# Kernel tuning notes

Measured on AMD Instinct MI355X. Metric: run time of the kernel, lower is better.

The kernel has to match this reference:

```python
import jax, jax.numpy as jnp
import numpy as np
import math

N = 512; D = 256; L = 6; H = 8; BINS = 64; LAM = 30.0; STEPS = 8; VOCAB = 20


def _pe(n, d):
    pos = jnp.arange(n, dtype=jnp.float32)[:, None]
    div = jnp.exp(jnp.arange(0, d, 2, dtype=jnp.float32) * (-math.log(10000.0) / d))
    pe = jnp.zeros((n, d), jnp.float32)
    pe = pe.at[:, 0::2].set(jnp.sin(pos * div))
    pe = pe.at[:, 1::2].set(jnp.cos(pos * div))
    return pe


def _ln(x, g, b, eps=1e-5):
    m = x.mean(-1, keepdims=True)
    v = x.var(-1, keepdims=True)
    return (x - m) / jnp.sqrt(v + eps) * g + b


def _gelu(x):
    return jax.nn.gelu(x, approximate=False)  # torch nn.GELU default (erf)


def setup_inputs() -> dict:
    key = jax.random.key(0)
    ks = jax.random.split(key, 20)
    s = 0.02
    nrm = lambda k, sh: jax.random.normal(k, sh, jnp.float32) * s
    z = lambda sh: jnp.zeros(sh, jnp.float32)
    o = lambda sh: jnp.ones(sh, jnp.float32)
    return {
        "tokens": jax.random.randint(ks[0], (1, N), 0, VOCAB),
        "emb": nrm(ks[1], (VOCAB, D)),
        "Wqkv": nrm(ks[2], (L, 3 * D, D)), "bqkv": z((L, 3 * D)),
        "Wo": nrm(ks[3], (L, D, D)), "bo": z((L, D)),
        "g1": o((L, D)), "be1": z((L, D)),
        "W1": nrm(ks[4], (L, 4 * D, D)), "b1": z((L, 4 * D)),
        "W2": nrm(ks[5], (L, D, 4 * D)), "b2": z((L, D)),
        "g2": o((L, D)), "be2": z((L, D)),
        "A1": nrm(ks[6], (D, D)), "a1b": z((D,)),
        "A2": nrm(ks[7], (1, D)), "a2b": z((1,)),
        "Cf": nrm(ks[8], (D, D)), "cb": z((D,)),
        "F1": nrm(ks[9], (D, 2 * D)), "f1b": z((D,)),
        "F2": nrm(ks[10], (BINS, D)), "f2b": z((BINS,)),
        "T1": nrm(ks[11], (D, D)), "t1b": z((D,)),
        "T2": nrm(ks[12], (2, D)), "t2b": z((2,)),
        "Cp": nrm(ks[13], (3, D)), "cpb": z((3,)),
        "noise": jax.random.normal(ks[14], (1, N, 3), jnp.float32),
    }


def reference(tokens, emb, Wqkv, bqkv, Wo, bo, g1, be1, W1, b1, W2, b2, g2, be2,
              A1, a1b, A2, a2b, Cf, cb, F1, f1b, F2, f2b, T1, t1b, T2, t2b,
              Cp, cpb, noise):
    x = emb[tokens] + _pe(N, D)  # [1,N,D]
    dh = D // H
    for l in range(L):  # post-norm TransformerEncoderLayer, ReLU activation
        qkv = x @ Wqkv[l].T + bqkv[l]  # [1,N,3D]
        q, k, v = jnp.split(qkv, 3, axis=-1)
        q = q.reshape(1, N, H, dh).transpose(0, 2, 1, 3)
        k = k.reshape(1, N, H, dh).transpose(0, 2, 1, 3)
        v = v.reshape(1, N, H, dh).transpose(0, 2, 1, 3)
        att = jax.nn.softmax(jnp.einsum('bhqd,bhkd->bhqk', q, k) / math.sqrt(dh), axis=-1)
        o = jnp.einsum('bhqk,bhkd->bhqd', att, v).transpose(0, 2, 1, 3).reshape(1, N, D)
        x = _ln(x + o @ Wo[l].T + bo[l], g1[l], be1[l])
        f = jax.nn.relu(x @ W1[l].T + b1[l]) @ W2[l].T + b2[l]
        x = _ln(x + f, g2[l], be2[l])
    latent = x
    # AdaptiveAlphaPredictor
    ah = _gelu(latent @ A1.T + a1b) @ A2.T + a2b  # [1,N,1]
    alpha = 1.2 + jax.nn.sigmoid(ah)[..., 0] * (3.5 - 1.2)  # [1,N]
    # CSOCRGAttention: power-law x exp-decay kernel over |i-j|
    idx = jnp.arange(N, dtype=jnp.float32)
    r = jnp.abs(idx[:, None] - idx[None, :]) + 1e-4  # [N,N]
    ap = (alpha[:, :, None] + alpha[:, None, :]) * 0.5  # [1,N,N]
    kern = r[None] ** (-ap) * jnp.exp(-r[None] / LAM)
    kern = kern / (kern.sum(-1, keepdims=True) + 1e-8)
    latent = jnp.einsum('bij,bjd->bid', kern, latent)
    # ContactPriorHead
    hh = latent @ Cf.T + cb
    contact = jax.nn.sigmoid(jnp.einsum('bid,bjd->bij', hh, hh))
    # DistogramHead: cat([xi, xj]) @ F1.T == xi @ F1[:, :D].T + xj @ F1[:, D:].T
    hi = latent @ F1[:, :D].T  # [1,N,D]
    hj = latent @ F1[:, D:].T  # [1,N,D]
    ph = _gelu(hi[:, :, None, :] + hj[:, None, :, :] + f1b)  # [1,N,N,D]
    disto = ph @ F2.T + f2b  # [1,N,N,BINS]
    # TorsionGenerator
    t = _gelu(latent @ T1.T + t1b) @ T2.T + t2b  # [1,N,2]
    phi = jnp.tanh(t[..., 0]) * jnp.pi
    psi = jnp.tanh(t[..., 1]) * jnp.pi
    # DiffusionInitializer: fixed small sequential refinement loop
    target = latent @ Cp.T + cpb  # [1,N,3]
    xc = noise
    for tt in reversed(range(STEPS)):
        a = (tt + 1) / STEPS
        xc = a * xc + (1.0 - a) * target
    return latent, alpha, contact, disto, phi, psi, xc


if __name__ == "__main__":
    outs = reference(**setup_inputs())
    for o in outs:
        print(o.shape, o.dtype)
```

## Files before the change

### kernel.cpp

```cpp
#include <hip/hip_runtime.h>
#include <hip/hip_bf16.h>

#define DEV __device__ __forceinline__

typedef float f32x4 __attribute__((ext_vector_type(4)));
typedef short short8 __attribute__((ext_vector_type(8)));
typedef short short4v __attribute__((ext_vector_type(4)));

DEV short f2bf(float f) {
    union { float f; unsigned u; } c; c.f = f;
    unsigned r = (c.u + 0x7FFFu + ((c.u >> 16) & 1u)) >> 16;
    return (short)r;
}

DEV short f2bf_n(float f) {
    __hip_bfloat16 b = __float2bfloat16(f);
    union { __hip_bfloat16 b; short s; } c; c.b = b;
    return c.s;
}

DEV float gelu_t(float x) {
    float x2 = x * x;
    float y = x * (0.7978845608f + 0.0356774081f * x2);
    float e = exp2f(-2.8853900817779268f * fabsf(y));
    float t = (1.f - e) * __frcp_rn(1.f + e);
    t = copysignf(t, y);
    return 0.5f * x * (1.f + t);
}

DEV float wred_sum(float v) {
    #pragma unroll
    for (int off = 1; off < 64; off <<= 1) v += __shfl_xor(v, off);
    return v;
}

struct CvtPack {
    const float* s[9];
    short* d[9];
    int n[9];
};
__global__ __launch_bounds__(256) void k_cvt_all(CvtPack p) {
    #pragma unroll 1
    for (int seg = 0; seg < 9; ++seg) {
        int n4 = p.n[seg] >> 2;
        const float4* src = (const float4*)p.s[seg];
        short4v* dst = (short4v*)p.d[seg];
        for (int i = blockIdx.x * 256 + threadIdx.x; i < n4; i += gridDim.x * 256) {
            float4 v = src[i];
            short4v o;
            o[0] = f2bf(v.x); o[1] = f2bf(v.y); o[2] = f2bf(v.z); o[3] = f2bf(v.w);
            dst[i] = o;
        }
    }
}

__global__ __launch_bounds__(256) void k_embed(const int* __restrict__ tokens,
                                               const float* __restrict__ emb,
                                               float* __restrict__ x,
                                               short* __restrict__ xb) {
    int n = blockIdx.x, d = threadIdx.x;
    int tok = tokens[n];
    float div = expf((float)((d >> 1) * 2) * -0.035977892079030837f);
    float arg = (float)n * div;
    float pe = (d & 1) ? cosf(arg) : sinf(arg);
    float v = emb[tok * 256 + d] + pe;
    x[n * 256 + d] = v;
    xb[n * 256 + d] = f2bf(v);
}

__global__ __launch_bounds__(64) void k_gemm16(const short* __restrict__ A,
                                               const short* __restrict__ W,
                                               const float* __restrict__ bias,
                                               float* __restrict__ outf,
                                               short* __restrict__ outb,
                                               short* __restrict__ vt,
                                               int M, int K, int ldw, int act) {
    int m0 = blockIdx.x * 16, n0 = blockIdx.y * 16;
    int lane = threadIdx.x;
    int cr = lane & 15, g = lane >> 4;
    const short* a0 = A + (size_t)(n0 + cr) * K + g * 8;
    const short* b0 = W + (size_t)(m0 + cr) * ldw + g * 8;
    f32x4 acc = {0.f, 0.f, 0.f, 0.f};
    #pragma unroll 8
    for (int k = 0; k < K; k += 32) {
        short8 av = *(const short8*)(a0 + k);
        short8 bv = *(const short8*)(b0 + k);
        acc = __builtin_amdgcn_mfma_f32_16x16x32_bf16(av, bv, acc, 0, 0, 0);
    }
    float bb = bias ? bias[m0 + cr] : 0.f;
    int m = m0 + cr;
    #pragma unroll
    for (int r = 0; r < 4; ++r) {
        int row = n0 + g * 4 + r;
        float v = acc[r] + bb;
        if (act == 1) v = fmaxf(v, 0.f);
        else if (act == 2) v = gelu_t(v);
        else if (act == 3) v = 1.f / (1.f + __expf(-v));
        if (outf) outf[(size_t)row * M + m] = v;
        if (outb) outb[(size_t)row * M + m] = f2bf(v);
        if (vt && m >= 512) vt[(size_t)(m - 512) * 512 + row] = f2bf(v);
    }
}

__global__ __launch_bounds__(64) void k_attn3(const short* __restrict__ qkvb,
                                              const short* __restrict__ vt,
                                              short* __restrict__ obuf_bf) {
    __shared__ __align__(16) short Pb[16][40];
    int h = blockIdx.x, qt = blockIdx.y;
    int lane = threadIdx.x;
    int cr = lane & 15, g = lane >> 4;
    int qb = qt * 16;
    short8 qf = *(const short8*)(qkvb + (size_t)(qb + cr) * 768 + h * 32 + g * 8);
    f32x4 s[32];
    #pragma unroll
    for (int jt = 0; jt < 32; ++jt) {
        short8 kf = *(const short8*)(qkvb + (size_t)(jt * 16 + cr) * 768 + 256 + h * 32 + g * 8);
        f32x4 z = {0.f, 0.f, 0.f, 0.f};
        s[jt] = __builtin_amdgcn_mfma_f32_16x16x32_bf16(qf, kf, z, 0, 0, 0);
    }
    const float sc = 0.17677669529663687f;
    float m[4], l[4];
    #pragma unroll
    for (int r = 0; r < 4; ++r) {
        float mm = -1e30f;
        #pragma unroll
        for (int jt = 0; jt < 32; ++jt) mm = fmaxf(mm, s[jt][r]);
        #pragma unroll
        for (int off = 1; off < 16; off <<= 1) mm = fmaxf(mm, __shfl_xor(mm, off));
        m[r] = mm * sc;
    }
    #pragma unroll
    for (int r = 0; r < 4; ++r) {
        float ll = 0.f;
        #pragma unroll
        for (int jt = 0; jt < 32; ++jt) {
            float p = __expf(s[jt][r] * sc - m[r]);
            s[jt][r] = p;
            ll += p;
        }
        #pragma unroll
        for (int off = 1; off < 16; off <<= 1) ll += __shfl_xor(ll, off);
        l[r] = ll;
    }
    const short* vth0 = vt + (size_t)(h * 32 + cr) * 512;
    const short* vth1 = vt + (size_t)(h * 32 + 16 + cr) * 512;
    f32x4 o0 = {0.f,0.f,0.f,0.f}, o1 = o0;
    #pragma unroll
    for (int c = 0; c < 16; ++c) {
        #pragma unroll
        for (int r = 0; r < 4; ++r) {
            Pb[4 * g + r][cr]      = f2bf(s[2 * c][r]);
            Pb[4 * g + r][16 + cr] = f2bf(s[2 * c + 1][r]);
        }
        short8 pa = *(const short8*)&Pb[cr][g * 8];
        short8 v0 = *(const short8*)(vth0 + c * 32 + g * 8);
        short8 v1 = *(const short8*)(vth1 + c * 32 + g * 8);
        o0 = __builtin_amdgcn_mfma_f32_16x16x32_bf16(pa, v0, o0, 0, 0, 0);
        o1 = __builtin_amdgcn_mfma_f32_16x16x32_bf16(pa, v1, o1, 0, 0, 0);
    }
    #pragma unroll
    for (int r = 0; r < 4; ++r) {
        float inv = 1.f / l[r];
        int q = qb + 4 * g + r;
        short* op = obuf_bf + (size_t)q * 256 + h * 32;
        op[cr]      = f2bf(o0[r] * inv);
        op[16 + cr] = f2bf(o1[r] * inv);
    }
}

__global__ __launch_bounds__(64) void k_ln(const float* xr, const float* y,
                                           const float* __restrict__ g,
                                           const float* __restrict__ b,
                                           float* out, short* outb) {
    int n = blockIdx.x, lane = threadIdx.x;
    float4 xv = *(const float4*)(xr + (size_t)n * 256 + lane * 4);
    float4 yv = *(const float4*)(y + (size_t)n * 256 + lane * 4);
    float t0 = xv.x + yv.x, t1 = xv.y + yv.y, t2 = xv.z + yv.z, t3 = xv.w + yv.w;
    float s = t0 + t1 + t2 + t3;
    float sq = t0 * t0 + t1 * t1 + t2 * t2 + t3 * t3;
    s = wred_sum(s);
    sq = wred_sum(sq);
    float mean = s * (1.f / 256.f);
    float var = sq * (1.f / 256.f) - mean * mean;
    float rstd = rsqrtf(var + 1e-5f);
    float4 gv = *(const float4*)(g + lane * 4);
    float4 bv = *(const float4*)(b + lane * 4);
    float r0 = (t0 - mean) * rstd * gv.x + bv.x;
    float r1 = (t1 - mean) * rstd * gv.y + bv.y;
    float r2 = (t2 - mean) * rstd * gv.z + bv.z;
    float r3 = (t3 - mean) * rstd * gv.w + bv.w;
    *(float4*)(out + (size_t)n * 256 + lane * 4) = make_float4(r0, r1, r2, r3);
    short4v ob; ob[0] = f2bf(r0); ob[1] = f2bf(r1); ob[2] = f2bf(r2); ob[3] = f2bf(r3);
    *(short4v*)(outb + (size_t)n * 256 + lane * 4) = ob;
}

__global__ __launch_bounds__(64) void k_alpha(const float* __restrict__ g,
                                              const float* __restrict__ A2,
                                              const float* __restrict__ a2b,
                                              float* __restrict__ alpha) {
    int n = blockIdx.x, lane = threadIdx.x;
    float4 gv = *(const float4*)(g + (size_t)n * 256 + lane * 4);
    float4 av = *(const float4*)(A2 + lane * 4);
    float s = gv.x * av.x + gv.y * av.y + gv.z * av.z + gv.w * av.w;
    s = wred_sum(s);
    if (lane == 0) {
        float ah = s + a2b[0];
        alpha[n] = 1.2f + 2.3f / (1.f + __expf(-ah));
    }
}

__global__ __launch_bounds__(256) void k_kern(const float* __restrict__ latent,
                                              const float* __restrict__ alpha,
                                              float* __restrict__ out,
                                              short* __restrict__ outb) {
    __shared__ float wl[512];
    __shared__ float partial[4];
    int i = blockIdx.x, t = threadIdx.x;
    float ai = alpha[i];
    float w0, w1;
    {
        int j = t;
        float dd = fabsf((float)(i - j)) + 1e-4f;
        float ap = 0.5f * (ai + alpha[j]);
        w0 = exp2f(-ap * __log2f(dd) - dd * 0.048089834696298776f);
        j = t + 256;
        dd = fabsf((float)(i - j)) + 1e-4f;
        ap = 0.5f * (ai + alpha[j]);
        w1 = exp2f(-ap * __log2f(dd) - dd * 0.048089834696298776f);
    }
    wl[t] = w0; wl[t + 256] = w1;
    float s = wred_sum(w0 + w1);
    if ((t & 63) == 0) partial[t >> 6] = s;
    __syncthreads();
    float S = partial[0] + partial[1] + partial[2] + partial[3];
    float inv = 1.f / (S + 1e-8f);
    float acc = 0.f;
    #pragma unroll 4
    for (int j = 0; j < 512; ++j) acc += wl[j] * latent[(size_t)j * 256 + t];
    float v = acc * inv;
    out[(size_t)i * 256 + t] = v;
    outb[(size_t)i * 256 + t] = f2bf(v);
}

__global__ __launch_bounds__(256) void k_disto3(const float* __restrict__ hi,
                                                const float* __restrict__ hj,
                                                const short* __restrict__ F2bf,
                                                const float* __restrict__ f2b,
                                                float* __restrict__ out) {
    __shared__ __align__(16) float hjs[16][260];
    int jt = blockIdx.x, it = blockIdx.y;
    int j0 = jt * 16;
    int t = threadIdx.x;
    for (int q = t; q < 1024; q += 256) {
        int r = q >> 6, c = (q & 63) << 2;
        float4 v = *(const float4*)(hj + (size_t)(j0 + r) * 256 + c);
        *(float4*)&hjs[r][c] = v;
    }
    __syncthreads();
    int w = t >> 6, lane = t & 63;
    int cr = lane & 15, g = lane >> 4;
    int i0 = it * 8 + w * 2;
    float bb[4];
    #pragma unroll
    for (int c = 0; c < 4; ++c) bb[c] = f2b[c * 16 + cr];
    f32x4 acc[2][4];
    #pragma unroll
    for (int ii = 0; ii < 2; ++ii)
        #pragma unroll
        for (int c = 0; c < 4; ++c) acc[ii][c] = (f32x4){0.f,0.f,0.f,0.f};
    #pragma unroll 1
    for (int ks = 0; ks < 8; ++ks) {
        int kb = ks * 32 + g * 8;
        short8 B[4];
        #pragma unroll
        for (int c = 0; c < 4; ++c)
            B[c] = *(const short8*)(F2bf + (size_t)(c * 16 + cr) * 256 + kb);
        float4 ja = *(const float4*)&hjs[cr][kb];
        float4 jb = *(const float4*)&hjs[cr][kb + 4];
        #pragma unroll
        for (int ii = 0; ii < 2; ++ii) {
            const float* hr = hi + (size_t)(i0 + ii) * 256 + kb;
            float4 ha = *(const float4*)(hr);
            float4 hb = *(const float4*)(hr + 4);
            short8 af;
            af[0] = f2bf_n(gelu_t(ha.x + ja.x));
            af[1] = f2bf_n(gelu_t(ha.y + ja.y));
            af[2] = f2bf_n(gelu_t(ha.z + ja.z));
            af[3] = f2bf_n(gelu_t(ha.w + ja.w));
            af[4] = f2bf_n(gelu_t(hb.x + jb.x));
            af[5] = f2bf_n(gelu_t(hb.y + jb.y));
            af[6] = f2bf_n(gelu_t(hb.z + jb.z));
            af[7] = f2bf_n(gelu_t(hb.w + jb.w));
            #pragma unroll
            for (int c = 0; c < 4; ++c)
                acc[ii][c] = __builtin_amdgcn_mfma_f32_16x16x32_bf16(af, B[c], acc[ii][c], 0, 0, 0);
        }
    }
    #pragma unroll
    for (int ii = 0; ii < 2; ++ii) {
        #pragma unroll
        for (int r = 0; r < 4; ++r) {
            int jl = g * 4 + r;
            float* op = out + ((size_t)(i0 + ii) * 512 + j0 + jl) * 64;
            op[cr]      = acc[ii][0][r] + bb[0];
            op[cr + 16] = acc[ii][1][r] + bb[1];
            op[cr + 32] = acc[ii][2][r] + bb[2];
            op[cr + 48] = acc[ii][3][r] + bb[3];
        }
    }
}

__global__ __launch_bounds__(64) void k_torsion(const float* __restrict__ g,
                                                const float* __restrict__ T2,
                                                const float* __restrict__ t2b,
                                                float* __restrict__ phi,
                                                float* __restrict__ psi) {
    int n = blockIdx.x, lane = threadIdx.x;
    float4 gv = *(const float4*)(g + (size_t)n * 256 + lane * 4);
    float4 w0 = *(const float4*)(T2 + lane * 4);
    float4 w1 = *(const float4*)(T2 + 256 + lane * 4);
    float s0 = gv.x * w0.x + gv.y * w0.y + gv.z * w0.z + gv.w * w0.w;
    float s1 = gv.x * w1.x + gv.y * w1.y + gv.z * w1.z + gv.w * w1.w;
    s0 = wred_sum(s0);
    s1 = wred_sum(s1);
    if (lane == 0) {
        phi[n] = tanhf(s0 + t2b[0]) * 3.14159265358979323846f;
        psi[n] = tanhf(s1 + t2b[1]) * 3.14159265358979323846f;
    }
}

__global__ __launch_bounds__(64) void k_diffusion(const float* __restrict__ latent,
                                                  const float* __restrict__ Cp,
                                                  const float* __restrict__ cpb,
                                                  const float* __restrict__ noise,
                                                  float* __restrict__ xc) {
    int n = blockIdx.x, lane = threadIdx.x;
    float4 lv = *(const float4*)(latent + (size_t)n * 256 + lane * 4);
    const float CN = 40320.0f / 16777216.0f;
    float s[3];
    #pragma unroll
    for (int c = 0; c < 3; ++c) {
        float4 w = *(const float4*)(Cp + c * 256 + lane * 4);
        float v = lv.x * w.x + lv.y * w.y + lv.z * w.z + lv.w * w.w;
        s[c] = wred_sum(v);
    }
    if (lane == 0) {
        #pragma unroll
        for (int c = 0; c < 3; ++c) {
            float tg = s[c] + cpb[c];
            xc[n * 3 + c] = CN * noise[n * 3 + c] + (1.f - CN) * tg;
        }
    }
}

extern "C" void kernel_launch(void* const* d_in, const int* in_sizes, int n_in,
                              void* d_out, int out_size, void* d_ws, size_t ws_size,
                              hipStream_t stream) {
    const int*   tokens = (const int*)d_in[0];
    const float* emb  = (const float*)d_in[1];
    const float* Wqkv = (const float*)d_in[2];
    const float* bqkv = (const float*)d_in[3];
    const float* Wo   = (const float*)d_in[4];
    const float* bo   = (const float*)d_in[5];
    const float* g1   = (const float*)d_in[6];
    const float* be1  = (const float*)d_in[7];
    const float* W1   = (const float*)d_in[8];
    const float* b1   = (const float*)d_in[9];
    const float* W2   = (const float*)d_in[10];
    const float* b2   = (const float*)d_in[11];
    const float* g2   = (const float*)d_in[12];
    const float* be2  = (const float*)d_in[13];
    const float* A1   = (const float*)d_in[14];
    const float* a1b  = (const float*)d_in[15];
    const float* A2   = (const float*)d_in[16];
    const float* a2b  = (const float*)d_in[17];
    const float* Cf   = (const float*)d_in[18];
    const float* cb   = (const float*)d_in[19];
    const float* F1   = (const float*)d_in[20];
    const float* f1b  = (const float*)d_in[21];
    const float* F2   = (const float*)d_in[22];
    const float* f2b  = (const float*)d_in[23];
    const float* T1   = (const float*)d_in[24];
    const float* t1b  = (const float*)d_in[25];
    const float* T2   = (const float*)d_in[26];
    const float* t2b  = (const float*)d_in[27];
    const float* Cp   = (const float*)d_in[28];
    const float* cpb  = (const float*)d_in[29];
    const float* noise= (const float*)d_in[30];

    float* ws   = (float*)d_ws;
    float* x    = ws;
    float* y2   = ws + 131072;
    float* gbuf = ws + 262144;
    float* hi   = ws + 393216;
    float* hj   = ws + 524288;
    short* S    = (short*)(ws + 655360);
    short* x_bf    = S;
    short* obuf_bf = S + 131072;
    short* h1_bf   = S + 262144;
    short* hh_bf   = S + 786432;
    short* lat_bf  = S + 917504;
    short* F2bf    = S + 1048576;
    short* qkv_bf  = S + 1064960;
    short* vt      = S + 1458176;
    short* Wqkv_bf = S + 1589248;
    short* Wo_bf   = S + 2768896;
    short* W1_bf   = S + 3162112;
    short* W2_bf   = S + 4734976;
    short* A1_bf   = S + 6307840;
    short* Cf_bf   = S + 6373376;
    short* F1_bf   = S + 6438912;
    short* T1_bf   = S + 6569984;

    float* out = (float*)d_out;
    float* o_latent  = out;
    float* o_alpha   = out + 131072;
    float* o_contact = out + 131584;
    float* o_disto   = out + 393728;
    float* o_phi     = out + 17170944;
    float* o_psi     = out + 17171456;
    float* o_xc      = out + 17171968;

    CvtPack p;
    p.s[0] = Wqkv; p.d[0] = Wqkv_bf; p.n[0] = 1179648;
    p.s[1] = Wo;   p.d[1] = Wo_bf;   p.n[1] = 393216;
    p.s[2] = W1;   p.d[2] = W1_bf;   p.n[2] = 1572864;
    p.s[3] = W2;   p.d[3] = W2_bf;   p.n[3] = 1572864;
    p.s[4] = A1;   p.d[4] = A1_bf;   p.n[4] = 65536;
    p.s[5] = Cf;   p.d[5] = Cf_bf;   p.n[5] = 65536;
    p.s[6] = F1;   p.d[6] = F1_bf;   p.n[6] = 131072;
    p.s[7] = T1;   p.d[7] = T1_bf;   p.n[7] = 65536;
    p.s[8] = F2;   p.d[8] = F2bf;    p.n[8] = 16384;
    k_cvt_all<<<512, 256, 0, stream>>>(p);

    k_embed<<<512, 256, 0, stream>>>(tokens, emb, x, x_bf);

    for (int l = 0; l < 6; ++l) {
        k_gemm16<<<dim3(48, 32), 64, 0, stream>>>(x_bf, Wqkv_bf + (size_t)l * 196608,
            bqkv + l * 768, nullptr, qkv_bf, vt, 768, 256, 256, 0);
        k_attn3<<<dim3(8, 32), 64, 0, stream>>>(qkv_bf, vt, obuf_bf);
        k_gemm16<<<dim3(16, 32), 64, 0, stream>>>(obuf_bf, Wo_bf + (size_t)l * 65536,
            bo + l * 256, y2, nullptr, nullptr, 256, 256, 256, 0);
        k_ln<<<512, 64, 0, stream>>>(x, y2, g1 + l * 256, be1 + l * 256, x, x_bf);
        k_gemm16<<<dim3(64, 32), 64, 0, stream>>>(x_bf, W1_bf + (size_t)l * 262144,
            b1 + l * 1024, nullptr, h1_bf, nullptr, 1024, 256, 256, 1);
        k_gemm16<<<dim3(16, 32), 64, 0, stream>>>(h1_bf, W2_bf + (size_t)l * 262144,
            b2 + l * 256, y2, nullptr, nullptr, 256, 1024, 1024, 0);
        k_ln<<<512, 64, 0, stream>>>(x, y2, g2 + l * 256, be2 + l * 256, x, x_bf);
    }

    k_gemm16<<<dim3(16, 32), 64, 0, stream>>>(x_bf, A1_bf, a1b, gbuf, nullptr, nullptr,
                                              256, 256, 256, 2);
    k_alpha<<<512, 64, 0, stream>>>(gbuf, A2, a2b, o_alpha);
    k_kern<<<512, 256, 0, stream>>>(x, o_alpha, o_latent, lat_bf);
    k_gemm16<<<dim3(16, 32), 64, 0, stream>>>(lat_bf, Cf_bf, cb, nullptr, hh_bf, nullptr,
                                              256, 256, 256, 0);
    k_gemm16<<<dim3(32, 32), 64, 0, stream>>>(hh_bf, hh_bf, nullptr, o_contact, nullptr,
                                              nullptr, 512, 256, 256, 3);
    k_gemm16<<<dim3(16, 32), 64, 0, stream>>>(lat_bf, F1_bf, f1b, hi, nullptr, nullptr,
                                              256, 256, 512, 0);
    k_gemm16<<<dim3(16, 32), 64, 0, stream>>>(lat_bf, F1_bf + 256, nullptr, hj, nullptr,
                                              nullptr, 256, 256, 512, 0);
    k_disto3<<<dim3(32, 64), 256, 0, stream>>>(hi, hj, F2bf, f2b, o_disto);
    k_gemm16<<<dim3(16, 32), 64, 0, stream>>>(lat_bf, T1_bf, t1b, gbuf, nullptr, nullptr,
                                              256, 256, 256, 2);
    k_torsion<<<512, 64, 0, stream>>>(gbuf, T2, t2b, o_phi, o_psi);
    k_diffusion<<<512, 64, 0, stream>>>(o_latent, Cp, cpb, noise, o_xc);
}
```

Baseline: 389.8 us.

## Fuse Wo+LayerNorm and FFN+LayerNorm kernels, speed up GELU and bf16 packing

```diff
diff --git a/kernel.cpp b/kernel.cpp
--- a/kernel.cpp
+++ b/kernel.cpp
@@ -6,6 +6,17 @@
 typedef float f32x4 __attribute__((ext_vector_type(4)));
 typedef short short8 __attribute__((ext_vector_type(8)));
 typedef short short4v __attribute__((ext_vector_type(4)));
+
+#if __has_builtin(__builtin_amdgcn_exp2f)
+#define EXP2F __builtin_amdgcn_exp2f
+#else
+#define EXP2F exp2f
+#endif
+#if __has_builtin(__builtin_amdgcn_rcpf)
+#define RCPF __builtin_amdgcn_rcpf
+#else
+#define RCPF(x) (1.f / (x))
+#endif
 
 DEV short f2bf(float f) {
     union { float f; unsigned u; } c; c.f = f;
@@ -13,24 +24,30 @@
     return (short)r;
 }
 
-DEV short f2bf_n(float f) {
-    __hip_bfloat16 b = __float2bfloat16(f);
-    union { __hip_bfloat16 b; short s; } c; c.b = b;
-    return c.s;
-}
-
-DEV float gelu_t(float x) {
+DEV int cvt_pk_bf16(float lo, float hi) {
+    int d;
+    asm("v_cvt_pk_bf16_f32 %0, %1, %2" : "=v"(d) : "v"(lo), "v"(hi));
+    return d;
+}
+
+DEV float gelu_fast(float x) {
     float x2 = x * x;
-    float y = x * (0.7978845608f + 0.0356774081f * x2);
-    float e = exp2f(-2.8853900817779268f * fabsf(y));
-    float t = (1.f - e) * __frcp_rn(1.f + e);
-    t = copysignf(t, y);
+    float y = x * __builtin_fmaf(0.0356774081f, x2, 0.7978845608f);
+    y = fminf(fmaxf(y, -15.f), 15.f);
+    float e = EXP2F(y * 2.8853900817779268f);
+    float r = RCPF(e + 1.f);
+    float t = (e - 1.f) * r;
     return 0.5f * x * (1.f + t);
 }
 
 DEV float wred_sum(float v) {
     #pragma unroll
     for (int off = 1; off < 64; off <<= 1) v += __shfl_xor(v, off);
+    return v;
+}
+DEV float red16(float v) {
+    #pragma unroll
+    for (int off = 1; off < 16; off <<= 1) v += __shfl_xor(v, off);
     return v;
 }
 
@@ -94,7 +111,7 @@
         int row = n0 + g * 4 + r;
         float v = acc[r] + bb;
         if (act == 1) v = fmaxf(v, 0.f);
-        else if (act == 2) v = gelu_t(v);
+        else if (act == 2) v = gelu_fast(v);
         else if (act == 3) v = 1.f / (1.f + __expf(-v));
         if (outf) outf[(size_t)row * M + m] = v;
         if (outb) outb[(size_t)row * M + m] = f2bf(v);
@@ -168,30 +185,145 @@
     }
 }
 
-__global__ __launch_bounds__(64) void k_ln(const float* xr, const float* y,
-                                           const float* __restrict__ g,
-                                           const float* __restrict__ b,
-                                           float* out, short* outb) {
-    int n = blockIdx.x, lane = threadIdx.x;
-    float4 xv = *(const float4*)(xr + (size_t)n * 256 + lane * 4);
-    float4 yv = *(const float4*)(y + (size_t)n * 256 + lane * 4);
-    float t0 = xv.x + yv.x, t1 = xv.y + yv.y, t2 = xv.z + yv.z, t3 = xv.w + yv.w;
-    float s = t0 + t1 + t2 + t3;
-    float sq = t0 * t0 + t1 * t1 + t2 * t2 + t3 * t3;
-    s = wred_sum(s);
-    sq = wred_sum(sq);
-    float mean = s * (1.f / 256.f);
-    float var = sq * (1.f / 256.f) - mean * mean;
-    float rstd = rsqrtf(var + 1e-5f);
-    float4 gv = *(const float4*)(g + lane * 4);
-    float4 bv = *(const float4*)(b + lane * 4);
-    float r0 = (t0 - mean) * rstd * gv.x + bv.x;
-    float r1 = (t1 - mean) * rstd * gv.y + bv.y;
-    float r2 = (t2 - mean) * rstd * gv.z + bv.z;
-    float r3 = (t3 - mean) * rstd * gv.w + bv.w;
-    *(float4*)(out + (size_t)n * 256 + lane * 4) = make_float4(r0, r1, r2, r3);
-    short4v ob; ob[0] = f2bf(r0); ob[1] = f2bf(r1); ob[2] = f2bf(r2); ob[3] = f2bf(r3);
-    *(short4v*)(outb + (size_t)n * 256 + lane * 4) = ob;
+__global__ __launch_bounds__(512) void k_wo_ln(const short* __restrict__ obuf_bf,
+                                               const short* __restrict__ Wo_bf,
+                                               const float* __restrict__ bo,
+                                               const float* __restrict__ xres,
+                                               const float* __restrict__ gam,
+                                               const float* __restrict__ bet,
+                                               float* __restrict__ x_out,
+                                               short* __restrict__ xb_out) {
+    __shared__ float redS[16][8];
+    __shared__ float redQ[16][8];
+    int n0 = blockIdx.x * 16;
+    int t = threadIdx.x, w = t >> 6, lane = t & 63;
+    int cr = lane & 15, g = lane >> 4;
+    const short* a0 = obuf_bf + (size_t)(n0 + cr) * 256 + g * 8;
+    float tv[2][4];
+    #pragma unroll
+    for (int tt = 0; tt < 2; ++tt) {
+        int m0 = w * 32 + tt * 16;
+        const short* b0 = Wo_bf + (size_t)(m0 + cr) * 256 + g * 8;
+        f32x4 a = {0.f, 0.f, 0.f, 0.f};
+        #pragma unroll
+        for (int k = 0; k < 256; k += 32) {
+            a = __builtin_amdgcn_mfma_f32_16x16x32_bf16(*(const short8*)(a0 + k),
+                                                        *(const short8*)(b0 + k), a, 0, 0, 0);
+        }
+        float bb = bo[m0 + cr];
+        #pragma unroll
+        for (int r = 0; r < 4; ++r) {
+            int row = n0 + g * 4 + r;
+            tv[tt][r] = a[r] + bb + xres[(size_t)row * 256 + m0 + cr];
+        }
+    }
+    #pragma unroll
+    for (int r = 0; r < 4; ++r) {
+        float s = tv[0][r] + tv[1][r];
+        float q = tv[0][r] * tv[0][r] + tv[1][r] * tv[1][r];
+        s = red16(s);
+        q = red16(q);
+        if (cr == 0) { redS[g * 4 + r][w] = s; redQ[g * 4 + r][w] = q; }
+    }
+    __syncthreads();
+    #pragma unroll
+    for (int r = 0; r < 4; ++r) {
+        int row = g * 4 + r;
+        float S = 0.f, Q = 0.f;
+        #pragma unroll
+        for (int j = 0; j < 8; ++j) { S += redS[row][j]; Q += redQ[row][j]; }
+        float mean = S * (1.f / 256.f);
+        float var = Q * (1.f / 256.f) - mean * mean;
+        float rstd = rsqrtf(var + 1e-5f);
+        int grow = n0 + row;
+        #pragma unroll
+        for (int tt = 0; tt < 2; ++tt) {
+            int mm = w * 32 + tt * 16 + cr;
+            float o = (tv[tt][r] - mean) * rstd * gam[mm] + bet[mm];
+            x_out[(size_t)grow * 256 + mm] = o;
+            xb_out[(size_t)grow * 256 + mm] = f2bf(o);
+        }
+    }
+}
+
+__global__ __launch_bounds__(512) void k_ffn_ln(const short* __restrict__ x_bf,
+                                                const short* __restrict__ W1_bf,
+                                                const float* __restrict__ b1,
+                                                const short* __restrict__ W2_bf,
+                                                const float* __restrict__ b2,
+                                                const float* __restrict__ xres,
+                                                const float* __restrict__ gam,
+                                                const float* __restrict__ bet,
+                                                float* __restrict__ x_out,
+                                                short* __restrict__ xb_out) {
+    __shared__ short h1s[16][1032];
+    __shared__ float redS[16][8];
+    __shared__ float redQ[16][8];
+    int n0 = blockIdx.x * 16;
+    int t = threadIdx.x, w = t >> 6, lane = t & 63;
+    int cr = lane & 15, g = lane >> 4;
+    const short* a0 = x_bf + (size_t)(n0 + cr) * 256 + g * 8;
+    #pragma unroll 1
+    for (int u = 0; u < 8; ++u) {
+        int m0 = w * 128 + u * 16;
+        const short* b0 = W1_bf + (size_t)(m0 + cr) * 256 + g * 8;
+        f32x4 a = {0.f, 0.f, 0.f, 0.f};
+        #pragma unroll
+        for (int k = 0; k < 256; k += 32) {
+            a = __builtin_amdgcn_mfma_f32_16x16x32_bf16(*(const short8*)(a0 + k),
+                                                        *(const short8*)(b0 + k), a, 0, 0, 0);
+        }
+        float bb = b1[m0 + cr];
+        #pragma unroll
+        for (int r = 0; r < 4; ++r)
+            h1s[g * 4 + r][m0 + cr] = f2bf(fmaxf(a[r] + bb, 0.f));
+    }
+    __syncthreads();
+    float tv[2][4];
+    #pragma unroll
+    for (int tt = 0; tt < 2; ++tt) {
+        int m0 = w * 32 + tt * 16;
+        const short* b0 = W2_bf + (size_t)(m0 + cr) * 1024 + g * 8;
+        f32x4 a = {0.f, 0.f, 0.f, 0.f};
+        #pragma unroll 8
+        for (int k = 0; k < 1024; k += 32) {
+            a = __builtin_amdgcn_mfma_f32_16x16x32_bf16(*(const short8*)&h1s[cr][k + g * 8],
+                                                        *(const short8*)(b0 + k), a, 0, 0, 0);
+        }
+        float bb = b2[m0 + cr];
+        #pragma unroll
+        for (int r = 0; r < 4; ++r) {
+            int row = n0 + g * 4 + r;
+            tv[tt][r] = a[r] + bb + xres[(size_t)row * 256 + m0 + cr];
+        }
+    }
+    #pragma unroll
+    for (int r = 0; r < 4; ++r) {
+        float s = tv[0][r] + tv[1][r];
+        float q = tv[0][r] * tv[0][r] + tv[1][r] * tv[1][r];
+        s = red16(s);
+        q = red16(q);
+        if (cr == 0) { redS[g * 4 + r][w] = s; redQ[g * 4 + r][w] = q; }
+    }
+    __syncthreads();
+    #pragma unroll
+    for (int r = 0; r < 4; ++r) {
+        int row = g * 4 + r;
+        float S = 0.f, Q = 0.f;
+        #pragma unroll
+        for (int j = 0; j < 8; ++j) { S += redS[row][j]; Q += redQ[row][j]; }
+        float mean = S * (1.f / 256.f);
+        float var = Q * (1.f / 256.f) - mean * mean;
+        float rstd = rsqrtf(var + 1e-5f);
+        int grow = n0 + row;
+        #pragma unroll
+        for (int tt = 0; tt < 2; ++tt) {
+            int mm = w * 32 + tt * 16 + cr;
+            float o = (tv[tt][r] - mean) * rstd * gam[mm] + bet[mm];
+            x_out[(size_t)grow * 256 + mm] = o;
+            xb_out[(size_t)grow * 256 + mm] = f2bf(o);
+        }
+    }
 }
 
 __global__ __launch_bounds__(64) void k_alpha(const float* __restrict__ g,
@@ -242,7 +374,7 @@
     outb[(size_t)i * 256 + t] = f2bf(v);
 }
 
-__global__ __launch_bounds__(256) void k_disto3(const float* __restrict__ hi,
+__global__ __launch_bounds__(256) void k_disto4(const float* __restrict__ hi,
                                                 const float* __restrict__ hj,
                                                 const short* __restrict__ F2bf,
                                                 const float* __restrict__ f2b,
@@ -253,8 +385,7 @@
     int t = threadIdx.x;
     for (int q = t; q < 1024; q += 256) {
         int r = q >> 6, c = (q & 63) << 2;
-        float4 v = *(const float4*)(hj + (size_t)(j0 + r) * 256 + c);
-        *(float4*)&hjs[r][c] = v;
+        *(float4*)&hjs[r][c] = *(const float4*)(hj + (size_t)(j0 + r) * 256 + c);
     }
     __syncthreads();
     int w = t >> 6, lane = t & 63;
@@ -282,18 +413,22 @@
             const float* hr = hi + (size_t)(i0 + ii) * 256 + kb;
             float4 ha = *(const float4*)(hr);
             float4 hb = *(const float4*)(hr + 4);
-            short8 af;
-            af[0] = f2bf_n(gelu_t(ha.x + ja.x));
-            af[1] = f2bf_n(gelu_t(ha.y + ja.y));
-            af[2] = f2bf_n(gelu_t(ha.z + ja.z));
-            af[3] = f2bf_n(gelu_t(ha.w + ja.w));
-            af[4] = f2bf_n(gelu_t(hb.x + jb.x));
-            af[5] = f2bf_n(gelu_t(hb.y + jb.y));
-            af[6] = f2bf_n(gelu_t(hb.z + jb.z));
-            af[7] = f2bf_n(gelu_t(hb.w + jb.w));
+            float p0 = gelu_fast(ha.x + ja.x);
+            float p1 = gelu_fast(ha.y + ja.y);
+            float p2 = gelu_fast(ha.z + ja.z);
+            float p3 = gelu_fast(ha.w + ja.w);
+            float p4 = gelu_fast(hb.x + jb.x);
+            float p5 = gelu_fast(hb.y + jb.y);
+            float p6 = gelu_fast(hb.z + jb.z);
+            float p7 = gelu_fast(hb.w + jb.w);
+            union { int i[4]; short8 s; } u;
+            u.i[0] = cvt_pk_bf16(p0, p1);
+            u.i[1] = cvt_pk_bf16(p2, p3);
+            u.i[2] = cvt_pk_bf16(p4, p5);
+            u.i[3] = cvt_pk_bf16(p6, p7);
             #pragma unroll
             for (int c = 0; c < 4; ++c)
-                acc[ii][c] = __builtin_amdgcn_mfma_f32_16x16x32_bf16(af, B[c], acc[ii][c], 0, 0, 0);
+                acc[ii][c] = __builtin_amdgcn_mfma_f32_16x16x32_bf16(u.s, B[c], acc[ii][c], 0, 0, 0);
         }
     }
     #pragma unroll
@@ -390,27 +525,25 @@
 
     float* ws   = (float*)d_ws;
     float* x    = ws;
-    float* y2   = ws + 131072;
-    float* gbuf = ws + 262144;
-    float* hi   = ws + 393216;
-    float* hj   = ws + 524288;
-    short* S    = (short*)(ws + 655360);
+    float* gbuf = ws + 131072;
+    float* hi   = ws + 262144;
+    float* hj   = ws + 393216;
+    short* S    = (short*)(ws + 524288);
     short* x_bf    = S;
     short* obuf_bf = S + 131072;
-    short* h1_bf   = S + 262144;
-    short* hh_bf   = S + 786432;
-    short* lat_bf  = S + 917504;
-    short* F2bf    = S + 1048576;
-    short* qkv_bf  = S + 1064960;
-    short* vt      = S + 1458176;
-    short* Wqkv_bf = S + 1589248;
-    short* Wo_bf   = S + 2768896;
-    short* W1_bf   = S + 3162112;
-    short* W2_bf   = S + 4734976;
-    short* A1_bf   = S + 6307840;
-    short* Cf_bf   = S + 6373376;
-    short* F1_bf   = S + 6438912;
-    short* T1_bf   = S + 6569984;
+    short* hh_bf   = S + 262144;
+    short* lat_bf  = S + 393216;
+    short* F2bf    = S + 524288;
+    short* qkv_bf  = S + 540672;
+    short* vt      = S + 933888;
+    short* Wqkv_bf = S + 1064960;
+    short* Wo_bf   = S + 2244608;
+    short* W1_bf   = S + 2637824;
+    short* W2_bf   = S + 4210688;
+    short* A1_bf   = S + 5783552;
+    short* Cf_bf   = S + 5849088;
+    short* F1_bf   = S + 5914624;
+    short* T1_bf   = S + 6045696;
 
     float* out = (float*)d_out;
     float* o_latent  = out;
@@ -439,14 +572,11 @@
         k_gemm16<<<dim3(48, 32), 64, 0, stream>>>(x_bf, Wqkv_bf + (size_t)l * 196608,
             bqkv + l * 768, nullptr, qkv_bf, vt, 768, 256, 256, 0);
         k_attn3<<<dim3(8, 32), 64, 0, stream>>>(qkv_bf, vt, obuf_bf);
-        k_gemm16<<<dim3(16, 32), 64, 0, stream>>>(obuf_bf, Wo_bf + (size_t)l * 65536,
-            bo + l * 256, y2, nullptr, nullptr, 256, 256, 256, 0);
-        k_ln<<<512, 64, 0, stream>>>(x, y2, g1 + l * 256, be1 + l * 256, x, x_bf);
-        k_gemm16<<<dim3(64, 32), 64, 0, stream>>>(x_bf, W1_bf + (size_t)l * 262144,
-            b1 + l * 1024, nullptr, h1_bf, nullptr, 1024, 256, 256, 1);
-        k_gemm16<<<dim3(16, 32), 64, 0, stream>>>(h1_bf, W2_bf + (size_t)l * 262144,
-            b2 + l * 256, y2, nullptr, nullptr, 256, 1024, 1024, 0);
-        k_ln<<<512, 64, 0, stream>>>(x, y2, g2 + l * 256, be2 + l * 256, x, x_bf);
+        k_wo_ln<<<32, 512, 0, stream>>>(obuf_bf, Wo_bf + (size_t)l * 65536, bo + l * 256,
+                                        x, g1 + l * 256, be1 + l * 256, x, x_bf);
+        k_ffn_ln<<<32, 512, 0, stream>>>(x_bf, W1_bf + (size_t)l * 262144, b1 + l * 1024,
+                                         W2_bf + (size_t)l * 262144, b2 + l * 256,
+                                         x, g2 + l * 256, be2 + l * 256, x, x_bf);
     }
 
     k_gemm16<<<dim3(16, 32), 64, 0, stream>>>(x_bf, A1_bf, a1b, gbuf, nullptr, nullptr,
@@ -461,7 +591,7 @@
                                               256, 256, 512, 0);
     k_gemm16<<<dim3(16, 32), 64, 0, stream>>>(lat_bf, F1_bf + 256, nullptr, hj, nullptr,
                                               nullptr, 256, 256, 512, 0);
-    k_disto3<<<dim3(32, 64), 256, 0, stream>>>(hi, hj, F2bf, f2b, o_disto);
+    k_disto4<<<dim3(32, 64), 256, 0, stream>>>(hi, hj, F2bf, f2b, o_disto);
     k_gemm16<<<dim3(16, 32), 64, 0, stream>>>(lat_bf, T1_bf, t1b, gbuf, nullptr, nullptr,
                                               256, 256, 256, 2);
     k_torsion<<<512, 64, 0, stream>>>(gbuf, T2, t2b, o_phi, o_psi);
```

Measured after the change: 476.0 us. 1.22x slower.
